# Kernel tuning notes

Hardware: AMD Instinct MI355X
Metric: run time of the kernel (lower is better)

## Reference

```python
import jax, jax.numpy as jnp
import numpy as np

N, D0, D1, D2 = 8192, 512, 256, 64


def setup_inputs() -> dict:
    key = jax.random.key(0)
    k1, k2, k3, k4 = jax.random.split(key, 4)
    xi = jax.random.normal(k1, (N, D0), dtype=jnp.float32)
    # graph filter ~ row-normalized adjacency: nonnegative, entries O(1/N)
    filter_matrix = jax.random.uniform(k2, (N, N), dtype=jnp.float32) * (2.0 / N)
    b1 = np.sqrt(6.0 / (D0 + D1))
    b2 = np.sqrt(6.0 / (D1 + D2))
    w1 = jax.random.uniform(k3, (D0, D1), dtype=jnp.float32, minval=-b1, maxval=b1)
    w2 = jax.random.uniform(k4, (D1, D2), dtype=jnp.float32, minval=-b2, maxval=b2)
    return {"xi": xi, "filter_matrix": filter_matrix, "w1": w1, "w2": w2}


def reference(xi, filter_matrix, w1, w2):
    # two GCN layers: F @ (X @ W)
    h = jax.nn.relu(filter_matrix @ (xi @ w1))          # [N, D1]
    emb = filter_matrix @ (h @ w2)                       # [N, D2]
    # pairwise squared Euclidean distances between rows of emb -> [N, N]
    sq = jnp.sum(emb * emb, axis=1)                      # [N]
    dists = jnp.maximum(sq[:, None] + sq[None, :] - 2.0 * (emb @ emb.T), 0.0)
    recons_w = jax.nn.softmax(-dists, axis=1)            # row softmax of negative distances
    return emb, recons_w + 1e-10
```

## Files before the change

kernel.cpp:

```cpp
#include <hip/hip_runtime.h>

typedef short s16x8 __attribute__((ext_vector_type(8)));
typedef float f32x4 __attribute__((ext_vector_type(4)));
typedef unsigned int u32;

#define DEV static __device__ __forceinline__

DEV unsigned short f2bf(float x){
  u32 u = __builtin_bit_cast(u32, x);
  return (unsigned short)((u + 0x7FFFu + ((u >> 16) & 1u)) >> 16);
}
DEV float bf2f(unsigned short h){ u32 u = ((u32)h) << 16; return __builtin_bit_cast(float, u); }
DEV u32 pack2(float a, float b){ return (u32)f2bf(a) | ((u32)f2bf(b) << 16); }

DEV void gld16(const void* g, void* l){
  __builtin_amdgcn_global_load_lds((const __attribute__((address_space(1))) u32*)g,
                                   (__attribute__((address_space(3))) u32*)l, 16, 0, 0);
}

template<int N> DEV void vmwait(){
  static_assert(N>=0 && N<=8, "vmcnt range");
  if constexpr (N==0) asm volatile("s_waitcnt vmcnt(0)" ::: "memory");
  else if constexpr (N==1) asm volatile("s_waitcnt vmcnt(1)" ::: "memory");
  else if constexpr (N==2) asm volatile("s_waitcnt vmcnt(2)" ::: "memory");
  else if constexpr (N==3) asm volatile("s_waitcnt vmcnt(3)" ::: "memory");
  else if constexpr (N==4) asm volatile("s_waitcnt vmcnt(4)" ::: "memory");
  else if constexpr (N==5) asm volatile("s_waitcnt vmcnt(5)" ::: "memory");
  else if constexpr (N==6) asm volatile("s_waitcnt vmcnt(6)" ::: "memory");
  else if constexpr (N==7) asm volatile("s_waitcnt vmcnt(7)" ::: "memory");
  else                     asm volatile("s_waitcnt vmcnt(8)" ::: "memory");
}
DEV void pipebar(){
  __builtin_amdgcn_sched_barrier(0);
  __builtin_amdgcn_s_barrier();
  __builtin_amdgcn_sched_barrier(0);
}

__global__ void k_cvt(const float* __restrict__ src, unsigned short* __restrict__ dst, long n4){
  long i = (long)blockIdx.x*256 + threadIdx.x;
  long stride = (long)gridDim.x*256;
  for (; i < n4; i += stride){
    float4 v = ((const float4*)src)[i];
    int2 p; p.x = (int)pack2(v.x, v.y); p.y = (int)pack2(v.z, v.w);
    ((int2*)dst)[i] = p;
  }
}

__global__ void k_prep(const float* __restrict__ w1, const float* __restrict__ w2,
                       unsigned short* __restrict__ w1t, unsigned short* __restrict__ w2t){
  int idx = blockIdx.x*256 + threadIdx.x;
  if (idx < 512*256){ int r=idx/256, c=idx%256; w1t[(size_t)c*512 + r] = f2bf(w1[idx]); }
  else { int j = idx - 512*256; if (j < 256*64){ int r=j/64, c=j%64; w2t[(size_t)c*256 + r] = f2bf(w2[j]); } }
}

template<int ROWS,int BK,int THREADS>
DEV void stage_lds(const unsigned short* __restrict__ src, int row0, int ld,
                   int kk, char* lds, int tid){
  constexpr int SLOTS = BK/8, SLM = SLOTS-1, RPC = 64/SLOTS;
  constexpr int RSH = (SLOTS==4) ? 1 : 0;
  constexpr int NCH = ROWS*BK*2/1024;
  constexpr int NW = THREADS/64, NI = NCH/NW;
  static_assert(NI*NW==NCH, "chunk exact");
  const int lane = tid & 63, wid = tid >> 6;
  #pragma unroll
  for (int i=0;i<NI;i++){
    int c = i*NW + wid;
    int r = c*RPC + lane/SLOTS;
    int s = lane & SLM;
    int ks = s ^ ((r>>RSH)&SLM);
    gld16(src + (size_t)(row0+r)*ld + kk + ks*8, lds + c*1024);
  }
}

template<int BM,int BN,int BK,int WR,int WC,bool PART>
__global__ __launch_bounds__(WR*WC*64, (WR*WC>=8)?4:2)
void k_gemm(const unsigned short* __restrict__ A, const unsigned short* __restrict__ B,
            void* __restrict__ Cp, int lda, int ldb, int ldc, int kchunk, long pstride)
{
  constexpr int THREADS = WR*WC*64;
  constexpr int ROWB = BK*2, SLOTS = BK/8, SLM = SLOTS-1;
  constexpr int RSH = (SLOTS==4) ? 1 : 0;
  constexpr int TBYTES = (BM+BN)*ROWB;
  constexpr int WM = BM/WR, WN = BN/WC;
  constexpr int FM = WM/16, FN = WN/16, KS = BK/32;
  constexpr int LA = BM*ROWB/1024/(THREADS/64);
  constexpr int LB = BN*ROWB/1024/(THREADS/64);
  constexpr int L  = LA + LB;

  __shared__ char smem[3*TBYTES];

  const int tid = threadIdx.x, lane = tid & 63;
  const int wid = tid >> 6, wrr = wid / WC, wcc = wid % WC;
  const int m0 = blockIdx.y * BM, n0 = blockIdx.x * BN;
  const int kbeg = blockIdx.z * kchunk, nk = kchunk / BK;

  f32x4 acc[FM][FN];
  f32x4 z4 = {0.f,0.f,0.f,0.f};
  #pragma unroll
  for (int m=0;m<FM;m++)
    #pragma unroll
    for (int n=0;n<FN;n++) acc[m][n] = z4;

  auto stage = [&](int kk, char* buf){
    stage_lds<BM,BK,THREADS>(A, m0, lda, kk, buf, tid);
    stage_lds<BN,BK,THREADS>(B, n0, ldb, kk, buf + BM*ROWB, tid);
  };
  auto compute = [&](const char* buf){
    const char* bA = buf;
    const char* bB = buf + BM*ROWB;
    #pragma unroll
    for (int ks=0;ks<KS;ks++){
      s16x8 av[FM], bv[FN];
      #pragma unroll
      for (int m=0;m<FM;m++){
        int r = wrr*WM + m*16 + (lane&15);
        int s = (ks*4 + (lane>>4)) ^ ((r>>RSH)&SLM);
        av[m] = *(const s16x8*)(bA + r*ROWB + s*16);
      }
      #pragma unroll
      for (int n=0;n<FN;n++){
        int r = wcc*WN + n*16 + (lane&15);
        int s = (ks*4 + (lane>>4)) ^ ((r>>RSH)&SLM);
        bv[n] = *(const s16x8*)(bB + r*ROWB + s*16);
      }
      #pragma unroll
      for (int m=0;m<FM;m++)
        #pragma unroll
        for (int n=0;n<FN;n++)
          acc[m][n] = __builtin_amdgcn_mfma_f32_16x16x32_bf16(av[m], bv[n], acc[m][n], 0, 0, 0);
    }
  };

  char* bc  = smem;
  char* bn_ = smem + TBYTES;
  char* bf_ = smem + 2*TBYTES;

  stage(kbeg, bc);
  stage(kbeg + BK, bn_);

  for (int t=0; t<nk; t++){
    if (t+1 < nk) vmwait<L>();
    else          vmwait<0>();
    pipebar();
    if (t+2 < nk) stage(kbeg + (t+2)*BK, bf_);
    compute(bc);
    pipebar();
    char* tmp = bc; bc = bn_; bn_ = bf_; bf_ = tmp;
  }

  if constexpr (PART) {
    float* Cf = (float*)Cp + (size_t)blockIdx.z * pstride;
    #pragma unroll
    for (int m=0;m<FM;m++)
      #pragma unroll
      for (int n=0;n<FN;n++)
        #pragma unroll
        for (int r=0;r<4;r++){
          int row = m0 + wrr*WM + m*16 + (lane>>4)*4 + r;
          int col = n0 + wcc*WN + n*16 + (lane&15);
          Cf[(size_t)row*ldc + col] = acc[m][n][r];
        }
  } else {
    unsigned short* Ch = (unsigned short*)Cp;
    #pragma unroll
    for (int m=0;m<FM;m++)
      #pragma unroll
      for (int n=0;n<FN;n++)
        #pragma unroll
        for (int r=0;r<4;r++){
          int row = m0 + wrr*WM + m*16 + (lane>>4)*4 + r;
          int col = n0 + wcc*WN + n*16 + (lane&15);
          Ch[(size_t)row*ldc + col] = f2bf(acc[m][n][r]);
        }
  }
}

__global__ void k_hred(const float* __restrict__ hp, unsigned short* __restrict__ h){
  const long N = (long)8192*256/4;
  long i = (long)blockIdx.x*256 + threadIdx.x;
  if (i >= N) return;
  float4 s = ((const float4*)hp)[i];
  #pragma unroll
  for (int z=1; z<8; z++){
    float4 v = ((const float4*)(hp + (size_t)z*8192*256))[i];
    s.x+=v.x; s.y+=v.y; s.z+=v.z; s.w+=v.w;
  }
  int2 p;
  p.x = (int)pack2(fmaxf(s.x,0.f), fmaxf(s.y,0.f));
  p.y = (int)pack2(fmaxf(s.z,0.f), fmaxf(s.w,0.f));
  ((int2*)h)[i] = p;
}

__global__ void k_emb_fin(const float* __restrict__ ep, float* __restrict__ emb_out,
                          unsigned short* __restrict__ embb, float* __restrict__ sq){
  int idx = blockIdx.x*256 + threadIdx.x;
  float v = 0.f;
  #pragma unroll
  for (int z=0; z<8; z++) v += ep[(size_t)z*8192*64 + idx];
  emb_out[idx] = v;
  unsigned short ub = f2bf(v);
  embb[idx] = ub;
  float x = bf2f(ub);
  float s = x*x;
  #pragma unroll
  for (int off=32; off>0; off>>=1) s += __shfl_xor(s, off, 64);
  if ((threadIdx.x & 63)==0) sq[idx>>6] = s;
}

template<int PASS>
__global__ __launch_bounds__(256)
void k_dist(const unsigned short* __restrict__ embb, const float* __restrict__ sq,
            float* __restrict__ S, float* __restrict__ out)
{
  constexpr int ROWB = 128, SLM = 7;
  __shared__ char smem[2*128*128];
  char* bufA = smem;
  char* bufB = smem + 128*ROWB;
  const int tid=threadIdx.x, lane=tid&63, wid=tid>>6;
  const int wrr = wid>>1, wcc = wid&1;
  const int i0 = blockIdx.y*128, j0 = blockIdx.x*128;

  #pragma unroll
  for (int i=0;i<4;i++){
    int u = tid + i*256;
    int r = u>>3, c = u&7;
    int byte = r*ROWB + ((c^(r&SLM))*16);
    *(int4*)(bufA+byte) = *(const int4*)(embb + (size_t)(i0+r)*64 + c*8);
    *(int4*)(bufB+byte) = *(const int4*)(embb + (size_t)(j0+r)*64 + c*8);
  }
  __syncthreads();

  f32x4 acc[4][4];
  f32x4 z4 = {0.f,0.f,0.f,0.f};
  #pragma unroll
  for (int m=0;m<4;m++)
    #pragma unroll
    for (int n=0;n<4;n++) acc[m][n]=z4;

  #pragma unroll
  for (int ks=0;ks<2;ks++){
    s16x8 av[4], bv[4];
    #pragma unroll
    for (int m=0;m<4;m++){
      int r = wrr*64 + m*16 + (lane&15);
      int slot = (ks*4 + (lane>>4)) ^ (r&SLM);
      av[m] = *(const s16x8*)(bufA + r*ROWB + slot*16);
    }
    #pragma unroll
    for (int n=0;n<4;n++){
      int r = wcc*64 + n*16 + (lane&15);
      int slot = (ks*4 + (lane>>4)) ^ (r&SLM);
      bv[n] = *(const s16x8*)(bufB + r*ROWB + slot*16);
    }
    #pragma unroll
    for (int m=0;m<4;m++)
      #pragma unroll
      for (int n=0;n<4;n++)
        acc[m][n] = __builtin_amdgcn_mfma_f32_16x16x32_bf16(av[m], bv[n], acc[m][n], 0, 0, 0);
  }

  float sqj[4];
  #pragma unroll
  for (int n=0;n<4;n++) sqj[n] = sq[j0 + wcc*64 + n*16 + (lane&15)];

  #pragma unroll
  for (int m=0;m<4;m++){
    #pragma unroll
    for (int r=0;r<4;r++){
      int row = i0 + wrr*64 + m*16 + (lane>>4)*4 + r;
      float sqi = sq[row];
      if constexpr (PASS==1){
        float v = 0.f;
        #pragma unroll
        for (int n=0;n<4;n++){
          float d = fmaxf(sqi + sqj[n] - 2.f*acc[m][n][r], 0.f);
          v += __expf(-d);
        }
        #pragma unroll
        for (int off=1; off<16; off<<=1) v += __shfl_xor(v, off, 64);
        if ((lane&15)==0) atomicAdd(S+row, v);
      } else {
        float inv = 1.0f / S[row];
        #pragma unroll
        for (int n=0;n<4;n++){
          int col = j0 + wcc*64 + n*16 + (lane&15);
          float d = fmaxf(sqi + sqj[n] - 2.f*acc[m][n][r], 0.f);
          out[(size_t)row*8192 + col] = __expf(-d)*inv + 1e-10f;
        }
      }
    }
  }
}

extern "C" void kernel_launch(void* const* d_in, const int* in_sizes, int n_in,
                              void* d_out, int out_size, void* d_ws, size_t ws_size,
                              hipStream_t stream)
{
  const float* xi = (const float*)d_in[0];
  const float* F  = (const float*)d_in[1];
  const float* w1 = (const float*)d_in[2];
  const float* w2 = (const float*)d_in[3];
  float* out = (float*)d_out;
  float* emb_out = out;
  float* recons  = out + (size_t)8192*64;

  unsigned short* Fb = (unsigned short*)recons;

  char* ws = (char*)d_ws;
  size_t off = 0;
  auto alloc = [&](size_t bytes)->char*{ char* p = ws + off; off += (bytes + 255) & ~(size_t)255; return p; };
  unsigned short* w1t  = (unsigned short*)alloc((size_t)256*512*2);
  unsigned short* w2t  = (unsigned short*)alloc((size_t)64*256*2);
  unsigned short* xib  = (unsigned short*)alloc((size_t)8192*512*2);
  unsigned short* t1t  = (unsigned short*)alloc((size_t)256*8192*2);
  unsigned short* t2t  = (unsigned short*)alloc((size_t)64*8192*2);
  unsigned short* h    = (unsigned short*)alloc((size_t)8192*256*2);
  unsigned short* embb = (unsigned short*)alloc((size_t)8192*64*2);
  float* sq     = (float*)alloc((size_t)8192*4);
  float* h_part = (float*)alloc((size_t)8*8192*256*4);
  float* e_part = (float*)alloc((size_t)8*8192*64*4);
  float* S      = (float*)alloc((size_t)8192*4);

  hipMemsetAsync(S, 0, (size_t)8192*4, stream);

  k_prep<<<dim3((512*256 + 256*64)/256), 256, 0, stream>>>(w1, w2, w1t, w2t);
  k_cvt<<<dim3(2048),256,0,stream>>>(F,  Fb,  (long)8192*8192/4);
  k_cvt<<<dim3(256), 256,0,stream>>>(xi, xib, (long)8192*512/4);

  k_gemm<128,64,64,2,2,false><<<dim3(128,2,1),256,0,stream>>>(
      w1t, xib, t1t, 512, 512, 8192, 512, 0);

  k_gemm<128,256,32,2,4,true><<<dim3(1,64,8),512,0,stream>>>(
      Fb, t1t, h_part, 8192, 8192, 256, 1024, (long)8192*256);

  k_hred<<<dim3(2048),256,0,stream>>>(h_part, h);

  k_gemm<64,32,64,2,2,false><<<dim3(256,1,1),256,0,stream>>>(
      w2t, h, t2t, 256, 256, 8192, 256, 0);

  k_gemm<128,64,64,2,2,true><<<dim3(1,64,8),256,0,stream>>>(
      Fb, t2t, e_part, 8192, 8192, 64, 1024, (long)8192*64);

  k_emb_fin<<<dim3(8192*64/256),256,0,stream>>>(e_part, emb_out, embb, sq);

  k_dist<1><<<dim3(64,64),256,0,stream>>>(embb, sq, S, recons);
  k_dist<2><<<dim3(64,64),256,0,stream>>>(embb, sq, S, recons);
}
```

Baseline: 348.1 us.

## Merge prep kernels and overlap F conversion with the first GEMM

Folds the weight transpose and xi conversion into one launch, and runs the X@W1 GEMM (retiled to 64x64) in the same launch as the large F fp32-to-bf16 conversion, so the two share the GPU instead of running back to back. The conversion loop is unrolled four ways to keep more loads in flight, and the F@t2 GEMM now uses 8 waves per block. This cuts launch count and overlaps compute-bound and bandwidth-bound work. The cost is a heterogeneous block mix whose LDS and occupancy are sized for the GEMM, plus changed launch bounds.

After: 368.4 us. 1.06x slower.

```diff
diff --git a/kernel.cpp b/kernel.cpp
--- a/kernel.cpp
+++ b/kernel.cpp
@@ -36,21 +36,43 @@
   __builtin_amdgcn_sched_barrier(0);
 }
 
-__global__ void k_cvt(const float* __restrict__ src, unsigned short* __restrict__ dst, long n4){
-  long i = (long)blockIdx.x*256 + threadIdx.x;
-  long stride = (long)gridDim.x*256;
+DEV void cvt_body(const float* __restrict__ src, unsigned short* __restrict__ dst,
+                  long n4, int bid, int nblocks){
+  long i = (long)bid*256 + threadIdx.x;
+  long stride = (long)nblocks*256;
+  for (; i + 3*stride < n4; i += 4*stride){
+    float4 v0 = ((const float4*)src)[i];
+    float4 v1 = ((const float4*)src)[i+stride];
+    float4 v2 = ((const float4*)src)[i+2*stride];
+    float4 v3 = ((const float4*)src)[i+3*stride];
+    int2 p0{(int)pack2(v0.x,v0.y),(int)pack2(v0.z,v0.w)};
+    int2 p1{(int)pack2(v1.x,v1.y),(int)pack2(v1.z,v1.w)};
+    int2 p2{(int)pack2(v2.x,v2.y),(int)pack2(v2.z,v2.w)};
+    int2 p3{(int)pack2(v3.x,v3.y),(int)pack2(v3.z,v3.w)};
+    ((int2*)dst)[i] = p0;
+    ((int2*)dst)[i+stride] = p1;
+    ((int2*)dst)[i+2*stride] = p2;
+    ((int2*)dst)[i+3*stride] = p3;
+  }
   for (; i < n4; i += stride){
     float4 v = ((const float4*)src)[i];
-    int2 p; p.x = (int)pack2(v.x, v.y); p.y = (int)pack2(v.z, v.w);
+    int2 p{(int)pack2(v.x,v.y),(int)pack2(v.z,v.w)};
     ((int2*)dst)[i] = p;
   }
 }
 
-__global__ void k_prep(const float* __restrict__ w1, const float* __restrict__ w2,
-                       unsigned short* __restrict__ w1t, unsigned short* __restrict__ w2t){
-  int idx = blockIdx.x*256 + threadIdx.x;
-  if (idx < 512*256){ int r=idx/256, c=idx%256; w1t[(size_t)c*512 + r] = f2bf(w1[idx]); }
-  else { int j = idx - 512*256; if (j < 256*64){ int r=j/64, c=j%64; w2t[(size_t)c*256 + r] = f2bf(w2[j]); } }
+__global__ __launch_bounds__(256)
+void k_misc(const float* __restrict__ w1, const float* __restrict__ w2,
+            unsigned short* __restrict__ w1t, unsigned short* __restrict__ w2t,
+            const float* __restrict__ xi, unsigned short* __restrict__ xib){
+  int bid = blockIdx.x;
+  if (bid < 576){
+    int idx = bid*256 + threadIdx.x;
+    if (idx < 512*256){ int r=idx/256, c=idx%256; w1t[(size_t)c*512 + r] = f2bf(w1[idx]); }
+    else { int j = idx - 512*256; if (j < 256*64){ int r=j/64, c=j%64; w2t[(size_t)c*256 + r] = f2bf(w2[j]); } }
+  } else {
+    cvt_body(xi, xib, (long)8192*512/4, bid-576, 512);
+  }
 }
 
 template<int ROWS,int BK,int THREADS>
@@ -73,9 +95,9 @@
 }
 
 template<int BM,int BN,int BK,int WR,int WC,bool PART>
-__global__ __launch_bounds__(WR*WC*64, (WR*WC>=8)?4:2)
-void k_gemm(const unsigned short* __restrict__ A, const unsigned short* __restrict__ B,
-            void* __restrict__ Cp, int lda, int ldb, int ldc, int kchunk, long pstride)
+DEV void gemm_body(const unsigned short* __restrict__ A, const unsigned short* __restrict__ B,
+                   void* __restrict__ Cp, int lda, int ldb, int ldc, int kchunk,
+                   long pstride, char* smem, int bx, int by, int bz)
 {
   constexpr int THREADS = WR*WC*64;
   constexpr int ROWB = BK*2, SLOTS = BK/8, SLM = SLOTS-1;
@@ -87,12 +109,10 @@
   constexpr int LB = BN*ROWB/1024/(THREADS/64);
   constexpr int L  = LA + LB;
 
-  __shared__ char smem[3*TBYTES];
-
   const int tid = threadIdx.x, lane = tid & 63;
   const int wid = tid >> 6, wrr = wid / WC, wcc = wid % WC;
-  const int m0 = blockIdx.y * BM, n0 = blockIdx.x * BN;
-  const int kbeg = blockIdx.z * kchunk, nk = kchunk / BK;
+  const int m0 = by * BM, n0 = bx * BN;
+  const int kbeg = bz * kchunk, nk = kchunk / BK;
 
   f32x4 acc[FM][FN];
   f32x4 z4 = {0.f,0.f,0.f,0.f};
@@ -149,7 +169,7 @@
   }
 
   if constexpr (PART) {
-    float* Cf = (float*)Cp + (size_t)blockIdx.z * pstride;
+    float* Cf = (float*)Cp + (size_t)bz * pstride;
     #pragma unroll
     for (int m=0;m<FM;m++)
       #pragma unroll
@@ -172,6 +192,31 @@
           int col = n0 + wcc*WN + n*16 + (lane&15);
           Ch[(size_t)row*ldc + col] = f2bf(acc[m][n][r]);
         }
+  }
+}
+
+template<int BM,int BN,int BK,int WR,int WC,bool PART>
+__global__ __launch_bounds__(WR*WC*64, 4)
+void k_gemm(const unsigned short* __restrict__ A, const unsigned short* __restrict__ B,
+            void* __restrict__ Cp, int lda, int ldb, int ldc, int kchunk, long pstride)
+{
+  __shared__ char smem[3*(BM+BN)*BK*2];
+  gemm_body<BM,BN,BK,WR,WC,PART>(A, B, Cp, lda, ldb, ldc, kchunk, pstride,
+                                 smem, blockIdx.x, blockIdx.y, blockIdx.z);
+}
+
+__global__ __launch_bounds__(256, 3)
+void k_big(const float* __restrict__ F, unsigned short* __restrict__ Fb,
+           const unsigned short* __restrict__ w1t, const unsigned short* __restrict__ xib,
+           unsigned short* __restrict__ t1t)
+{
+  __shared__ char smem[3*(64+64)*64*2];
+  int bid = blockIdx.x;
+  if (bid < 512){
+    gemm_body<64,64,64,2,2,false>(w1t, xib, t1t, 512, 512, 8192, 512, 0,
+                                  smem, bid % 128, bid / 128, 0);
+  } else {
+    cvt_body(F, Fb, (long)8192*8192/4, bid - 512, 2048);
   }
 }
 
@@ -323,12 +368,9 @@
 
   hipMemsetAsync(S, 0, (size_t)8192*4, stream);
 
-  k_prep<<<dim3((512*256 + 256*64)/256), 256, 0, stream>>>(w1, w2, w1t, w2t);
-  k_cvt<<<dim3(2048),256,0,stream>>>(F,  Fb,  (long)8192*8192/4);
-  k_cvt<<<dim3(256), 256,0,stream>>>(xi, xib, (long)8192*512/4);
-
-  k_gemm<128,64,64,2,2,false><<<dim3(128,2,1),256,0,stream>>>(
-      w1t, xib, t1t, 512, 512, 8192, 512, 0);
+  k_misc<<<dim3(1088),256,0,stream>>>(w1, w2, w1t, w2t, xi, xib);
+
+  k_big<<<dim3(2560),256,0,stream>>>(F, Fb, w1t, xib, t1t);
 
   k_gemm<128,256,32,2,4,true><<<dim3(1,64,8),512,0,stream>>>(
       Fb, t1t, h_part, 8192, 8192, 256, 1024, (long)8192*256);
@@ -338,7 +380,7 @@
   k_gemm<64,32,64,2,2,false><<<dim3(256,1,1),256,0,stream>>>(
       w2t, h, t2t, 256, 256, 8192, 256, 0);
 
-  k_gemm<128,64,64,2,2,true><<<dim3(1,64,8),256,0,stream>>>(
+  k_gemm<128,64,64,4,2,true><<<dim3(1,64,8),512,0,stream>>>(
       Fb, t2t, e_part, 8192, 8192, 64, 1024, (long)8192*64);
 
   k_emb_fin<<<dim3(8192*64/256),256,0,stream>>>(e_part, emb_out, embb, sq);
```
